# Performance work log

Hardware: AMD Instinct MI355X
Metric: run time of the kernel (lower is better)

The kernel has to match this reference:

```python
import jax, jax.numpy as jnp
import numpy as np

DIM = 768
HEADS = 12
HEAD_DIM = DIM // HEADS
HIDDEN = int(DIM * 4.0)
EPS = 1e-5


def _layernorm(x, g, b):
    mu = jnp.mean(x, axis=-1, keepdims=True)
    var = jnp.var(x, axis=-1, keepdims=True)
    return (x - mu) * jax.lax.rsqrt(var + EPS) * g + b


def setup_inputs() -> dict:
    key = jax.random.key(0)
    ks = jax.random.split(key, 12)
    s = 0.02
    return {
        "x": jax.random.normal(ks[0], (8, 1024, DIM), dtype=jnp.float32),
        "norm1_g": jnp.ones((DIM,), jnp.float32),
        "norm1_b": jnp.zeros((DIM,), jnp.float32),
        "qkv_w": jax.random.normal(ks[1], (3 * DIM, DIM), jnp.float32) * s,
        "qkv_b": jnp.zeros((3 * DIM,), jnp.float32),
        "proj_w": jax.random.normal(ks[2], (DIM, DIM), jnp.float32) * s,
        "proj_b": jnp.zeros((DIM,), jnp.float32),
        "norm2_g": jnp.ones((DIM,), jnp.float32),
        "norm2_b": jnp.zeros((DIM,), jnp.float32),
        "fc1_w": jax.random.normal(ks[3], (HIDDEN, DIM), jnp.float32) * s,
        "fc1_b": jnp.zeros((HIDDEN,), jnp.float32),
        "fc2_w": jax.random.normal(ks[4], (DIM, HIDDEN), jnp.float32) * s,
        "fc2_b": jnp.zeros((DIM,), jnp.float32),
    }


def reference(x, norm1_g, norm1_b, qkv_w, qkv_b, proj_w, proj_b,
              norm2_g, norm2_b, fc1_w, fc1_b, fc2_w, fc2_b):
    B, N, C = x.shape
    scale = HEAD_DIM ** -0.5

    # --- MHSA with pre-norm + residual ---
    h = _layernorm(x, norm1_g, norm1_b)
    qkv = h @ qkv_w.T + qkv_b                      # [B, N, 3C]
    qkv = qkv.reshape(B, N, 3, HEADS, HEAD_DIM)
    qkv = jnp.transpose(qkv, (2, 0, 3, 1, 4))      # [3, B, H, N, Dh]
    q, k, v = qkv[0], qkv[1], qkv[2]
    attn = jnp.einsum("bhnd,bhmd->bhnm", q, k) * scale
    attn = jax.nn.softmax(attn, axis=-1)
    o = jnp.einsum("bhnm,bhmd->bhnd", attn, v)     # [B, H, N, Dh]
    o = jnp.transpose(o, (0, 2, 1, 3)).reshape(B, N, C)
    x = x + (o @ proj_w.T + proj_b)

    # --- MLP with pre-norm + residual ---
    h = _layernorm(x, norm2_g, norm2_b)
    h = jax.nn.gelu(h @ fc1_w.T + fc1_b, approximate=False)
    x = x + (h @ fc2_w.T + fc2_b)
    return x
```

## Files before the change

kernel.cpp:

```cpp
#include <hip/hip_runtime.h>
#include <hip/hip_bf16.h>

typedef unsigned short u16;
using short8  = __attribute__((ext_vector_type(8))) short;
using floatx4 = __attribute__((ext_vector_type(4))) float;

__device__ inline u16 f2bu(float f) {
    __hip_bfloat16 h = __float2bfloat16(f);
    return __builtin_bit_cast(u16, h);
}
__device__ inline float b2f(u16 u) {
    unsigned v = (unsigned)u << 16;
    return __builtin_bit_cast(float, v);
}
__device__ inline float gelu_f(float v) {
    float u = 1.5957691216f * (v + 0.044715f * v * v * v);
    return v / (1.f + __expf(-u));
}

__device__ inline void load16(const u16* g, u16* l) {
    __builtin_amdgcn_global_load_lds(
        (const __attribute__((address_space(1))) void*)g,
        (__attribute__((address_space(3))) void*)l, 16, 0, 0);
}

__global__ void cvt_bf16v(const float4* __restrict__ in, ushort4* __restrict__ out, int n4) {
    int i = blockIdx.x * 256 + threadIdx.x;
    if (i < n4) {
        float4 f = in[i];
        ushort4 r;
        r.x = f2bu(f.x); r.y = f2bu(f.y); r.z = f2bu(f.z); r.w = f2bu(f.w);
        out[i] = r;
    }
}

__global__ __launch_bounds__(256) void layernorm_bf16(
    const float* __restrict__ x, const float* __restrict__ g,
    const float* __restrict__ b, u16* __restrict__ out)
{
    int row = blockIdx.x;
    int tid = threadIdx.x;
    const float* xr = x + (size_t)row * 768;
    float v0 = xr[tid], v1 = xr[tid + 256], v2 = xr[tid + 512];
    float s = v0 + v1 + v2;
    float ss = v0 * v0 + v1 * v1 + v2 * v2;
    for (int off = 1; off < 64; off <<= 1) {
        s  += __shfl_xor(s, off, 64);
        ss += __shfl_xor(ss, off, 64);
    }
    __shared__ float as[4], ass[4];
    int wave = tid >> 6, lane = tid & 63;
    if (lane == 0) { as[wave] = s; ass[wave] = ss; }
    __syncthreads();
    s  = as[0] + as[1] + as[2] + as[3];
    ss = ass[0] + ass[1] + ass[2] + ass[3];
    float mu  = s * (1.0f / 768.0f);
    float var = ss * (1.0f / 768.0f) - mu * mu;
    float rs  = rsqrtf(var + 1e-5f);
    u16* orow = out + (size_t)row * 768;
    orow[tid]       = f2bu((v0 - mu) * rs * g[tid]       + b[tid]);
    orow[tid + 256] = f2bu((v1 - mu) * rs * g[tid + 256] + b[tid + 256]);
    orow[tid + 512] = f2bu((v2 - mu) * rs * g[tid + 512] + b[tid + 512]);
}

__global__ __launch_bounds__(256) void red2(
    const ushort4* __restrict__ P0, const ushort4* __restrict__ P1,
    const float* __restrict__ bias, const float4* __restrict__ res,
    float4* __restrict__ out)
{
    int i = blockIdx.x * 256 + threadIdx.x;
    int col = (i % 192) * 4;
    ushort4 a = P0[i], b = P1[i];
    float4 o = res ? res[i] : out[i];
    o.x += bias[col + 0] + b2f(a.x) + b2f(b.x);
    o.y += bias[col + 1] + b2f(a.y) + b2f(b.y);
    o.z += bias[col + 2] + b2f(a.z) + b2f(b.z);
    o.w += bias[col + 3] + b2f(a.w) + b2f(b.w);
    out[i] = o;
}

__global__ __launch_bounds__(256) void red2_ln(
    const u16* __restrict__ P0, const u16* __restrict__ P1,
    const float* __restrict__ bias, const float* __restrict__ x,
    float* __restrict__ out,
    const float* __restrict__ g, const float* __restrict__ bb,
    u16* __restrict__ h)
{
    int row = blockIdx.x;
    int tid = threadIdx.x;
    size_t base = (size_t)row * 768;
    float v[3];
    float s = 0.f, ss = 0.f;
    #pragma unroll
    for (int j = 0; j < 3; ++j) {
        int col = tid + j * 256;
        size_t idx = base + col;
        float o = x[idx] + bias[col] + b2f(P0[idx]) + b2f(P1[idx]);
        out[idx] = o;
        v[j] = o;
        s += o; ss += o * o;
    }
    for (int off = 1; off < 64; off <<= 1) {
        s  += __shfl_xor(s, off, 64);
        ss += __shfl_xor(ss, off, 64);
    }
    __shared__ float as[4], ass[4];
    int wave = tid >> 6, lane = tid & 63;
    if (lane == 0) { as[wave] = s; ass[wave] = ss; }
    __syncthreads();
    s  = as[0] + as[1] + as[2] + as[3];
    ss = ass[0] + ass[1] + ass[2] + ass[3];
    float mu  = s * (1.0f / 768.0f);
    float var = ss * (1.0f / 768.0f) - mu * mu;
    float rs  = rsqrtf(var + 1e-5f);
    #pragma unroll
    for (int j = 0; j < 3; ++j) {
        int col = tid + j * 256;
        h[base + col] = f2bu((v[j] - mu) * rs * g[col] + bb[col]);
    }
}

__global__ __launch_bounds__(256) void gemm_k64(
    const u16* __restrict__ A, int lda,
    const u16* __restrict__ B, int ldb,
    int K,
    const float* __restrict__ bias,
    const float* __restrict__ res,
    float* __restrict__ outf, u16* __restrict__ outb,
    u16* __restrict__ parts, size_t pstride,
    int ldc, int act, int splits)
{
    __shared__ u16 lsa[128 * 64];
    __shared__ u16 lsb[128 * 64];

    int tid  = threadIdx.x;
    int wave = tid >> 6, lane = tid & 63;
    int quad = lane >> 4, l16 = lane & 15;
    int wrow = (wave >> 1) * 64;
    int wcol = (wave & 1) * 64;

    int gx = gridDim.x;
    int nblk = gx * gridDim.y;
    int flat = blockIdx.y * gx + blockIdx.x;
    int d = (flat & 7) * (nblk >> 3) + (flat >> 3);
    int m0 = (d / gx) * 128, n0 = (d % gx) * 128;

    int Kper = K / splits;
    int kbeg = blockIdx.z * Kper;

    floatx4 acc[4][4];
    for (int i = 0; i < 4; ++i)
        for (int j = 0; j < 4; ++j)
            acc[i][j] = (floatx4){0.f, 0.f, 0.f, 0.f};

    int rsub = lane >> 3;
    int gc   = (lane & 7) ^ rsub;
    const u16* gA[4];
    const u16* gB[4];
    #pragma unroll
    for (int j = 0; j < 4; ++j) {
        int r = (j * 4 + wave) * 8 + rsub;
        gA[j] = A + (size_t)(m0 + r) * lda + kbeg + gc * 8;
        gB[j] = B + (size_t)(n0 + r) * ldb + kbeg + gc * 8;
    }

    int xq0 = ((quad)     ^ (l16 & 7)) * 8;
    int xq1 = ((quad + 4) ^ (l16 & 7)) * 8;

    for (int k0 = 0; k0 < Kper; k0 += 64) {
        __syncthreads();
        #pragma unroll
        for (int j = 0; j < 4; ++j) {
            load16(gA[j], &lsa[(j * 4 + wave) * 512]);
            gA[j] += 64;
        }
        #pragma unroll
        for (int j = 0; j < 4; ++j) {
            load16(gB[j], &lsb[(j * 4 + wave) * 512]);
            gB[j] += 64;
        }
        __syncthreads();

        short8 af[4], bfr[4];
        #pragma unroll
        for (int rb = 0; rb < 4; ++rb) af[rb]  = *(short8*)&lsa[(wrow + rb * 16 + l16) * 64 + xq0];
        #pragma unroll
        for (int cb = 0; cb < 4; ++cb) bfr[cb] = *(short8*)&lsb[(wcol + cb * 16 + l16) * 64 + xq0];
        #pragma unroll
        for (int rb = 0; rb < 4; ++rb)
            #pragma unroll
            for (int cb = 0; cb < 4; ++cb)
                acc[rb][cb] = __builtin_amdgcn_mfma_f32_16x16x32_bf16(af[rb], bfr[cb], acc[rb][cb], 0, 0, 0);
        #pragma unroll
        for (int rb = 0; rb < 4; ++rb) af[rb]  = *(short8*)&lsa[(wrow + rb * 16 + l16) * 64 + xq1];
        #pragma unroll
        for (int cb = 0; cb < 4; ++cb) bfr[cb] = *(short8*)&lsb[(wcol + cb * 16 + l16) * 64 + xq1];
        #pragma unroll
        for (int rb = 0; rb < 4; ++rb)
            #pragma unroll
            for (int cb = 0; cb < 4; ++cb)
                acc[rb][cb] = __builtin_amdgcn_mfma_f32_16x16x32_bf16(af[rb], bfr[cb], acc[rb][cb], 0, 0, 0);
    }

    u16* pdst = (splits > 1) ? parts + (size_t)blockIdx.z * pstride : nullptr;
    #pragma unroll
    for (int rb = 0; rb < 4; ++rb)
        #pragma unroll
        for (int cb = 0; cb < 4; ++cb)
            #pragma unroll
            for (int r = 0; r < 4; ++r) {
                int row = m0 + wrow + rb * 16 + quad * 4 + r;
                int col = n0 + wcol + cb * 16 + l16;
                float v = acc[rb][cb][r];
                if (splits > 1) {
                    pdst[(size_t)row * ldc + col] = f2bu(v);
                } else {
                    v += bias[col];
                    if (res) v += res[(size_t)row * ldc + col];
                    if (act) v = gelu_f(v);
                    if (outf) outf[(size_t)row * ldc + col] = v;
                    else      outb[(size_t)row * ldc + col] = f2bu(v);
                }
            }
}

__global__ __launch_bounds__(256) void attn_fused(
    const u16* __restrict__ qkv, u16* __restrict__ o)
{
    const int N = 1024, C3 = 2304;
    int qb = blockIdx.x;
    int bh = blockIdx.y;
    int b = bh / 12, h = bh % 12;
    int tid = threadIdx.x, wave = tid >> 6, lane = tid & 63;
    int quad = lane >> 4, l16 = lane & 15;

    __shared__ u16 lk[64 * 64];
    __shared__ u16 lvt[64][72];
    __shared__ u16 lp[4][32][72];

    const size_t base = (size_t)b * N * C3;
    int q0 = qb * 128 + wave * 32;

    short8 qa[2][2];
    #pragma unroll
    for (int rb = 0; rb < 2; ++rb)
        #pragma unroll
        for (int ch = 0; ch < 2; ++ch)
            qa[rb][ch] = *(const short8*)&qkv[base + (size_t)(q0 + rb * 16 + l16) * C3 + h * 64 + ch * 32 + quad * 8];

    floatx4 oacc[2][4];
    #pragma unroll
    for (int i = 0; i < 2; ++i)
        #pragma unroll
        for (int j = 0; j < 4; ++j) oacc[i][j] = (floatx4){0.f, 0.f, 0.f, 0.f};
    float lsum[2][4] = {};

    for (int kt = 0; kt < N; kt += 64) {
        __syncthreads();
        #pragma unroll
        for (int i = 0; i < 2; ++i) {
            int idx = i * 2048 + wave * 512 + lane * 8;
            int r = idx >> 6;
            int gc = (lane & 7) ^ (r & 7);
            load16(&qkv[base + (size_t)(kt + r) * C3 + 768 + h * 64 + gc * 8], &lk[idx]);
        }
        {
            int key = tid & 63, dbase = (tid >> 6) * 16;
            const u16* vp = &qkv[base + (size_t)(kt + key) * C3 + 1536 + h * 64 + dbase];
            uint4 vv0 = *(const uint4*)vp;
            uint4 vv1 = *(const uint4*)(vp + 8);
            const u16* e0 = (const u16*)&vv0;
            const u16* e1 = (const u16*)&vv1;
            #pragma unroll
            for (int i = 0; i < 8; ++i) {
                lvt[dbase + i][key]     = e0[i];
                lvt[dbase + 8 + i][key] = e1[i];
            }
        }
        __syncthreads();

        #pragma unroll
        for (int kb = 0; kb < 4; ++kb) {
            int R = kb * 16 + l16;
            short8 b0 = *(short8*)&lk[R * 64 + ((quad ^ (R & 7)) * 8)];
            short8 b1 = *(short8*)&lk[R * 64 + (((quad + 4) ^ (R & 7)) * 8)];
            #pragma unroll
            for (int rb = 0; rb < 2; ++rb) {
                floatx4 c = (floatx4){0.f, 0.f, 0.f, 0.f};
                c = __builtin_amdgcn_mfma_f32_16x16x32_bf16(qa[rb][0], b0, c, 0, 0, 0);
                c = __builtin_amdgcn_mfma_f32_16x16x32_bf16(qa[rb][1], b1, c, 0, 0, 0);
                #pragma unroll
                for (int r = 0; r < 4; ++r) {
                    float p = __expf(c[r] * 0.125f);
                    lsum[rb][r] += p;
                    lp[wave][rb * 16 + quad * 4 + r][kb * 16 + l16] = f2bu(p);
                }
            }
        }

        short8 pa[2][2];
        #pragma unroll
        for (int rb = 0; rb < 2; ++rb) {
            pa[rb][0] = *(short8*)&lp[wave][rb * 16 + l16][quad * 8];
            pa[rb][1] = *(short8*)&lp[wave][rb * 16 + l16][32 + quad * 8];
        }
        #pragma unroll
        for (int db = 0; db < 4; ++db) {
            short8 vb0 = *(short8*)&lvt[db * 16 + l16][quad * 8];
            short8 vb1 = *(short8*)&lvt[db * 16 + l16][32 + quad * 8];
            #pragma unroll
            for (int rb = 0; rb < 2; ++rb) {
                oacc[rb][db] = __builtin_amdgcn_mfma_f32_16x16x32_bf16(pa[rb][0], vb0, oacc[rb][db], 0, 0, 0);
                oacc[rb][db] = __builtin_amdgcn_mfma_f32_16x16x32_bf16(pa[rb][1], vb1, oacc[rb][db], 0, 0, 0);
            }
        }
    }

    #pragma unroll
    for (int rb = 0; rb < 2; ++rb)
        #pragma unroll
        for (int r = 0; r < 4; ++r)
            for (int off = 1; off < 16; off <<= 1)
                lsum[rb][r] += __shfl_xor(lsum[rb][r], off, 64);

    #pragma unroll
    for (int rb = 0; rb < 2; ++rb)
        #pragma unroll
        for (int db = 0; db < 4; ++db)
            #pragma unroll
            for (int r = 0; r < 4; ++r) {
                int row = q0 + rb * 16 + quad * 4 + r;
                int col = h * 64 + db * 16 + l16;
                o[(size_t)(b * N + row) * 768 + col] = f2bu(oacc[rb][db][r] / lsum[rb][r]);
            }
}

extern "C" void kernel_launch(void* const* d_in, const int* in_sizes, int n_in,
                              void* d_out, int out_size, void* d_ws, size_t ws_size,
                              hipStream_t stream) {
    const float* x      = (const float*)d_in[0];
    const float* n1g    = (const float*)d_in[1];
    const float* n1b    = (const float*)d_in[2];
    const float* qkv_w  = (const float*)d_in[3];
    const float* qkv_b  = (const float*)d_in[4];
    const float* proj_w = (const float*)d_in[5];
    const float* proj_b = (const float*)d_in[6];
    const float* n2g    = (const float*)d_in[7];
    const float* n2b    = (const float*)d_in[8];
    const float* fc1_w  = (const float*)d_in[9];
    const float* fc1_b  = (const float*)d_in[10];
    const float* fc2_w  = (const float*)d_in[11];
    const float* fc2_b  = (const float*)d_in[12];
    float* out = (float*)d_out;

    const int T = 8192;
    char* ws = (char*)d_ws;
    u16* w_qkv  = (u16*)ws;               ws += (size_t)2304 * 768 * 2;
    u16* w_proj = (u16*)ws;               ws += (size_t)768 * 768 * 2;
    u16* w_fc1  = (u16*)ws;               ws += (size_t)3072 * 768 * 2;
    u16* w_fc2  = (u16*)ws;               ws += (size_t)768 * 3072 * 2;
    u16* h_buf  = (u16*)ws;               ws += (size_t)T * 768 * 2;
    u16* qkvbuf = (u16*)ws;               ws += (size_t)T * 2304 * 2;
    u16* o_buf  = (u16*)ws;               ws += (size_t)T * 768 * 2;
    u16* pbuf   = (u16*)ws;               ws += (size_t)T * 768 * 2;
    u16* fc1out = qkvbuf;
    bool do_split = (size_t)(ws - (char*)d_ws) <= ws_size;
    size_t pstr = (size_t)(pbuf - h_buf);

    cvt_bf16v<<<dim3(2304 * 768 / 4 / 256), 256, 0, stream>>>((const float4*)qkv_w,  (ushort4*)w_qkv,  2304 * 768 / 4);
    cvt_bf16v<<<dim3(768 * 768 / 4 / 256),  256, 0, stream>>>((const float4*)proj_w, (ushort4*)w_proj, 768 * 768 / 4);
    cvt_bf16v<<<dim3(3072 * 768 / 4 / 256), 256, 0, stream>>>((const float4*)fc1_w,  (ushort4*)w_fc1,  3072 * 768 / 4);
    cvt_bf16v<<<dim3(768 * 3072 / 4 / 256), 256, 0, stream>>>((const float4*)fc2_w,  (ushort4*)w_fc2,  768 * 3072 / 4);

    layernorm_bf16<<<dim3(T), 256, 0, stream>>>(x, n1g, n1b, h_buf);
    gemm_k64<<<dim3(2304 / 128, T / 128), 256, 0, stream>>>(
        h_buf, 768, w_qkv, 768, 768, qkv_b, nullptr, nullptr, qkvbuf, nullptr, 0, 2304, 0, 1);
    attn_fused<<<dim3(8, 96), 256, 0, stream>>>(qkvbuf, o_buf);
    if (do_split) {
        gemm_k64<<<dim3(768 / 128, T / 128, 2), 256, 0, stream>>>(
            o_buf, 768, w_proj, 768, 768, proj_b, nullptr, nullptr, nullptr,
            h_buf, pstr, 768, 0, 2);
        red2_ln<<<dim3(T), 256, 0, stream>>>(
            h_buf, pbuf, proj_b, x, out, n2g, n2b, h_buf);
    } else {
        gemm_k64<<<dim3(768 / 128, T / 128), 256, 0, stream>>>(
            o_buf, 768, w_proj, 768, 768, proj_b, x, out, nullptr, nullptr, 0, 768, 0, 1);
        layernorm_bf16<<<dim3(T), 256, 0, stream>>>(out, n2g, n2b, h_buf);
    }
    gemm_k64<<<dim3(3072 / 128, T / 128), 256, 0, stream>>>(
        h_buf, 768, w_fc1, 768, 768, fc1_b, nullptr, nullptr, fc1out, nullptr, 0, 3072, 1, 1);
    if (do_split) {
        gemm_k64<<<dim3(768 / 128, T / 128, 2), 256, 0, stream>>>(
            fc1out, 3072, w_fc2, 3072, 3072, fc2_b, nullptr, nullptr, nullptr,
            h_buf, pstr, 768, 0, 2);
        red2<<<dim3(T * 768 / 4 / 256), 256, 0, stream>>>(
            (const ushort4*)h_buf, (const ushort4*)pbuf, fc2_b, nullptr, (float4*)out);
    } else {
        gemm_k64<<<dim3(768 / 128, T / 128), 256, 0, stream>>>(
            fc1out, 3072, w_fc2, 3072, 3072, fc2_b, out, out, nullptr, nullptr, 0, 768, 0, 1);
    }
}
```

Measured before the change: 393.6 us.

## Double-buffer LDS tiles in GEMM and attention kernels with MFMA priority hints

Converts the GEMM and fused-attention main loops to a double-buffered LDS scheme: the next K/A/B tile is prefetched asynchronously into the alternate buffer while MFMAs run on the current one, which halves the barriers per iteration. In attention, V is loaded into registers early and transposed into LDS after compute. s_setprio hints are wrapped around the MFMA blocks to favour matrix issue. This doubles LDS usage (GEMM goes to 64KB), which may reduce occupancy, and it adds register pressure for the V prefetch.

```diff
diff --git a/kernel.cpp b/kernel.cpp
--- a/kernel.cpp
+++ b/kernel.cpp
@@ -130,8 +130,8 @@
     u16* __restrict__ parts, size_t pstride,
     int ldc, int act, int splits)
 {
-    __shared__ u16 lsa[128 * 64];
-    __shared__ u16 lsb[128 * 64];
+    __shared__ u16 lsa[2][128 * 64];
+    __shared__ u16 lsb[2][128 * 64];
 
     int tid  = threadIdx.x;
     int wave = tid >> 6, lane = tid & 63;
@@ -167,39 +167,50 @@
     int xq0 = ((quad)     ^ (l16 & 7)) * 8;
     int xq1 = ((quad + 4) ^ (l16 & 7)) * 8;
 
+    #pragma unroll
+    for (int j = 0; j < 4; ++j) { load16(gA[j], &lsa[0][(j * 4 + wave) * 512]); gA[j] += 64; }
+    #pragma unroll
+    for (int j = 0; j < 4; ++j) { load16(gB[j], &lsb[0][(j * 4 + wave) * 512]); gB[j] += 64; }
+    __syncthreads();
+
+    int cur = 0;
     for (int k0 = 0; k0 < Kper; k0 += 64) {
-        __syncthreads();
-        #pragma unroll
-        for (int j = 0; j < 4; ++j) {
-            load16(gA[j], &lsa[(j * 4 + wave) * 512]);
-            gA[j] += 64;
+        int nxt = cur ^ 1;
+        if (k0 + 64 < Kper) {
+            #pragma unroll
+            for (int j = 0; j < 4; ++j) { load16(gA[j], &lsa[nxt][(j * 4 + wave) * 512]); gA[j] += 64; }
+            #pragma unroll
+            for (int j = 0; j < 4; ++j) { load16(gB[j], &lsb[nxt][(j * 4 + wave) * 512]); gB[j] += 64; }
         }
-        #pragma unroll
-        for (int j = 0; j < 4; ++j) {
-            load16(gB[j], &lsb[(j * 4 + wave) * 512]);
-            gB[j] += 64;
-        }
-        __syncthreads();
-
+
+        const u16* la = lsa[cur];
+        const u16* lb = lsb[cur];
         short8 af[4], bfr[4];
         #pragma unroll
-        for (int rb = 0; rb < 4; ++rb) af[rb]  = *(short8*)&lsa[(wrow + rb * 16 + l16) * 64 + xq0];
-        #pragma unroll
-        for (int cb = 0; cb < 4; ++cb) bfr[cb] = *(short8*)&lsb[(wcol + cb * 16 + l16) * 64 + xq0];
+        for (int rb = 0; rb < 4; ++rb) af[rb]  = *(const short8*)&la[(wrow + rb * 16 + l16) * 64 + xq0];
+        #pragma unroll
+        for (int cb = 0; cb < 4; ++cb) bfr[cb] = *(const short8*)&lb[(wcol + cb * 16 + l16) * 64 + xq0];
+        __builtin_amdgcn_s_setprio(1);
         #pragma unroll
         for (int rb = 0; rb < 4; ++rb)
             #pragma unroll
             for (int cb = 0; cb < 4; ++cb)
                 acc[rb][cb] = __builtin_amdgcn_mfma_f32_16x16x32_bf16(af[rb], bfr[cb], acc[rb][cb], 0, 0, 0);
-        #pragma unroll
-        for (int rb = 0; rb < 4; ++rb) af[rb]  = *(short8*)&lsa[(wrow + rb * 16 + l16) * 64 + xq1];
-        #pragma unroll
-        for (int cb = 0; cb < 4; ++cb) bfr[cb] = *(short8*)&lsb[(wcol + cb * 16 + l16) * 64 + xq1];
+        __builtin_amdgcn_s_setprio(0);
+        #pragma unroll
+        for (int rb = 0; rb < 4; ++rb) af[rb]  = *(const short8*)&la[(wrow + rb * 16 + l16) * 64 + xq1];
+        #pragma unroll
+        for (int cb = 0; cb < 4; ++cb) bfr[cb] = *(const short8*)&lb[(wcol + cb * 16 + l16) * 64 + xq1];
+        __builtin_amdgcn_s_setprio(1);
         #pragma unroll
         for (int rb = 0; rb < 4; ++rb)
             #pragma unroll
             for (int cb = 0; cb < 4; ++cb)
                 acc[rb][cb] = __builtin_amdgcn_mfma_f32_16x16x32_bf16(af[rb], bfr[cb], acc[rb][cb], 0, 0, 0);
+        __builtin_amdgcn_s_setprio(0);
+
+        __syncthreads();
+        cur = nxt;
     }
 
     u16* pdst = (splits > 1) ? parts + (size_t)blockIdx.z * pstride : nullptr;
@@ -224,6 +235,37 @@
             }
 }
 
+__device__ inline void attn_stage_k(const u16* __restrict__ qkv, size_t base, int kt,
+                                    int h, int wave, int lane, u16* lkbuf)
+{
+    #pragma unroll
+    for (int i = 0; i < 2; ++i) {
+        int idx = i * 2048 + wave * 512 + lane * 8;
+        int r = idx >> 6;
+        int gc = (lane & 7) ^ (r & 7);
+        load16(&qkv[base + (size_t)(kt + r) * 2304 + 768 + h * 64 + gc * 8], &lkbuf[idx]);
+    }
+}
+__device__ inline void attn_load_v(const u16* __restrict__ qkv, size_t base, int kt,
+                                   int h, int tid, uint4& v0, uint4& v1)
+{
+    int key = tid & 63, dbase = (tid >> 6) * 16;
+    const u16* vp = &qkv[base + (size_t)(kt + key) * 2304 + 1536 + h * 64 + dbase];
+    v0 = *(const uint4*)vp;
+    v1 = *(const uint4*)(vp + 8);
+}
+__device__ inline void attn_write_v(int tid, const uint4& v0, const uint4& v1, u16 (*lvtbuf)[72])
+{
+    int key = tid & 63, dbase = (tid >> 6) * 16;
+    const u16* e0 = (const u16*)&v0;
+    const u16* e1 = (const u16*)&v1;
+    #pragma unroll
+    for (int i = 0; i < 8; ++i) {
+        lvtbuf[dbase + i][key]     = e0[i];
+        lvtbuf[dbase + 8 + i][key] = e1[i];
+    }
+}
+
 __global__ __launch_bounds__(256) void attn_fused(
     const u16* __restrict__ qkv, u16* __restrict__ o)
 {
@@ -234,8 +276,8 @@
     int tid = threadIdx.x, wave = tid >> 6, lane = tid & 63;
     int quad = lane >> 4, l16 = lane & 15;
 
-    __shared__ u16 lk[64 * 64];
-    __shared__ u16 lvt[64][72];
+    __shared__ u16 lk[2][64 * 64];
+    __shared__ u16 lvt[2][64][72];
     __shared__ u16 lp[4][32][72];
 
     const size_t base = (size_t)b * N * C3;
@@ -255,40 +297,37 @@
         for (int j = 0; j < 4; ++j) oacc[i][j] = (floatx4){0.f, 0.f, 0.f, 0.f};
     float lsum[2][4] = {};
 
+    attn_stage_k(qkv, base, 0, h, wave, lane, lk[0]);
+    {
+        uint4 a0, a1;
+        attn_load_v(qkv, base, 0, h, tid, a0, a1);
+        attn_write_v(tid, a0, a1, lvt[0]);
+    }
+    __syncthreads();
+
+    int cur = 0;
     for (int kt = 0; kt < N; kt += 64) {
-        __syncthreads();
-        #pragma unroll
-        for (int i = 0; i < 2; ++i) {
-            int idx = i * 2048 + wave * 512 + lane * 8;
-            int r = idx >> 6;
-            int gc = (lane & 7) ^ (r & 7);
-            load16(&qkv[base + (size_t)(kt + r) * C3 + 768 + h * 64 + gc * 8], &lk[idx]);
+        int nxt = cur ^ 1;
+        bool pf = (kt + 64) < N;
+        uint4 pv0, pv1;
+        if (pf) {
+            attn_stage_k(qkv, base, kt + 64, h, wave, lane, lk[nxt]);
+            attn_load_v(qkv, base, kt + 64, h, tid, pv0, pv1);
         }
-        {
-            int key = tid & 63, dbase = (tid >> 6) * 16;
-            const u16* vp = &qkv[base + (size_t)(kt + key) * C3 + 1536 + h * 64 + dbase];
-            uint4 vv0 = *(const uint4*)vp;
-            uint4 vv1 = *(const uint4*)(vp + 8);
-            const u16* e0 = (const u16*)&vv0;
-            const u16* e1 = (const u16*)&vv1;
-            #pragma unroll
-            for (int i = 0; i < 8; ++i) {
-                lvt[dbase + i][key]     = e0[i];
-                lvt[dbase + 8 + i][key] = e1[i];
-            }
-        }
-        __syncthreads();
-
+
+        const u16* lkc = lk[cur];
         #pragma unroll
         for (int kb = 0; kb < 4; ++kb) {
             int R = kb * 16 + l16;
-            short8 b0 = *(short8*)&lk[R * 64 + ((quad ^ (R & 7)) * 8)];
-            short8 b1 = *(short8*)&lk[R * 64 + (((quad + 4) ^ (R & 7)) * 8)];
+            short8 b0 = *(const short8*)&lkc[R * 64 + ((quad ^ (R & 7)) * 8)];
+            short8 b1 = *(const short8*)&lkc[R * 64 + (((quad + 4) ^ (R & 7)) * 8)];
             #pragma unroll
             for (int rb = 0; rb < 2; ++rb) {
                 floatx4 c = (floatx4){0.f, 0.f, 0.f, 0.f};
+                __builtin_amdgcn_s_setprio(1);
                 c = __builtin_amdgcn_mfma_f32_16x16x32_bf16(qa[rb][0], b0, c, 0, 0, 0);
                 c = __builtin_amdgcn_mfma_f32_16x16x32_bf16(qa[rb][1], b1, c, 0, 0, 0);
+                __builtin_amdgcn_s_setprio(0);
                 #pragma unroll
                 for (int r = 0; r < 4; ++r) {
                     float p = __expf(c[r] * 0.125f);
@@ -301,19 +340,25 @@
         short8 pa[2][2];
         #pragma unroll
         for (int rb = 0; rb < 2; ++rb) {
-            pa[rb][0] = *(short8*)&lp[wave][rb * 16 + l16][quad * 8];
-            pa[rb][1] = *(short8*)&lp[wave][rb * 16 + l16][32 + quad * 8];
+            pa[rb][0] = *(const short8*)&lp[wave][rb * 16 + l16][quad * 8];
+            pa[rb][1] = *(const short8*)&lp[wave][rb * 16 + l16][32 + quad * 8];
         }
         #pragma unroll
         for (int db = 0; db < 4; ++db) {
-            short8 vb0 = *(short8*)&lvt[db * 16 + l16][quad * 8];
-            short8 vb1 = *(short8*)&lvt[db * 16 + l16][32 + quad * 8];
+            short8 vb0 = *(const short8*)&lvt[cur][db * 16 + l16][quad * 8];
+            short8 vb1 = *(const short8*)&lvt[cur][db * 16 + l16][32 + quad * 8];
+            __builtin_amdgcn_s_setprio(1);
             #pragma unroll
             for (int rb = 0; rb < 2; ++rb) {
                 oacc[rb][db] = __builtin_amdgcn_mfma_f32_16x16x32_bf16(pa[rb][0], vb0, oacc[rb][db], 0, 0, 0);
                 oacc[rb][db] = __builtin_amdgcn_mfma_f32_16x16x32_bf16(pa[rb][1], vb1, oacc[rb][db], 0, 0, 0);
             }
+            __builtin_amdgcn_s_setprio(0);
         }
+
+        if (pf) attn_write_v(tid, pv0, pv1, lvt[nxt]);
+        __syncthreads();
+        cur = nxt;
     }
 
     #pragma unroll
```

New measurement: 447.8 us. +13.8%, slower.

## Double-buffer GEMM LDS tiles with K=32 stages and async prefetch

Applied to the files above, without the earlier changes.

The GEMM main loop now uses two LDS buffers with K-step 32 instead of a single K=64 buffer. The next tile is prefetched via global_load_lds while the current tile is consumed, and waits use vmcnt. The LDS layout packs two rows per 64-element line with an XOR swizzle. The goal is to overlap global loads with MFMA work. In exchange there are twice as many loop iterations and barriers, plus more complex LDS address arithmetic.

```diff
diff --git a/kernel.cpp b/kernel.cpp
--- a/kernel.cpp
+++ b/kernel.cpp
@@ -130,8 +130,7 @@
     u16* __restrict__ parts, size_t pstride,
     int ldc, int act, int splits)
 {
-    __shared__ u16 lsa[128 * 64];
-    __shared__ u16 lsb[128 * 64];
+    __shared__ u16 ls[2][2][64 * 64];
 
     int tid  = threadIdx.x;
     int wave = tid >> 6, lane = tid & 63;
@@ -147,60 +146,66 @@
 
     int Kper = K / splits;
     int kbeg = blockIdx.z * Kper;
+    int NT = Kper >> 5;
 
     floatx4 acc[4][4];
     for (int i = 0; i < 4; ++i)
         for (int j = 0; j < 4; ++j)
             acc[i][j] = (floatx4){0.f, 0.f, 0.f, 0.f};
 
-    int rsub = lane >> 3;
-    int gc   = (lane & 7) ^ rsub;
-    const u16* gA[4];
-    const u16* gB[4];
-    #pragma unroll
-    for (int j = 0; j < 4; ++j) {
-        int r = (j * 4 + wave) * 8 + rsub;
-        gA[j] = A + (size_t)(m0 + r) * lda + kbeg + gc * 8;
-        gB[j] = B + (size_t)(n0 + r) * ldb + kbeg + gc * 8;
-    }
-
-    int xq0 = ((quad)     ^ (l16 & 7)) * 8;
-    int xq1 = ((quad + 4) ^ (l16 & 7)) * 8;
-
-    for (int k0 = 0; k0 < Kper; k0 += 64) {
-        __syncthreads();
-        #pragma unroll
-        for (int j = 0; j < 4; ++j) {
-            load16(gA[j], &lsa[(j * 4 + wave) * 512]);
-            gA[j] += 64;
-        }
-        #pragma unroll
-        for (int j = 0; j < 4; ++j) {
-            load16(gB[j], &lsb[(j * 4 + wave) * 512]);
-            gB[j] += 64;
-        }
-        __syncthreads();
-
+    int rsub  = lane >> 3;
+    int gc    = (lane & 7) ^ rsub;
+    int ghalf = gc >> 2, gq = gc & 3;
+    const u16* gA[2];
+    const u16* gB[2];
+    #pragma unroll
+    for (int j = 0; j < 2; ++j) {
+        int r = ((j * 4 + wave) * 8 + rsub) * 2 + ghalf;
+        gA[j] = A + (size_t)(m0 + r) * lda + kbeg + gq * 8;
+        gB[j] = B + (size_t)(n0 + r) * ldb + kbeg + gq * 8;
+    }
+
+#define STAGE(bf_) do { \
+    _Pragma("unroll") \
+    for (int j_ = 0; j_ < 2; ++j_) { load16(gA[j_], &ls[bf_][0][(j_ * 4 + wave) * 512]); gA[j_] += 32; } \
+    _Pragma("unroll") \
+    for (int j_ = 0; j_ < 2; ++j_) { load16(gB[j_], &ls[bf_][1][(j_ * 4 + wave) * 512]); gB[j_] += 32; } \
+} while (0)
+
+    STAGE(0);
+
+    for (int c = 0; c < NT; ++c) {
+        int bc = c & 1;
+        __builtin_amdgcn_s_barrier();
+        if (c + 1 < NT) {
+            STAGE(bc ^ 1);
+            asm volatile("s_waitcnt vmcnt(4)" ::: "memory");
+        } else {
+            asm volatile("s_waitcnt vmcnt(0)" ::: "memory");
+        }
+        __builtin_amdgcn_s_barrier();
+        __builtin_amdgcn_sched_barrier(0);
+
+        const u16* la = ls[bc][0];
+        const u16* lb = ls[bc][1];
         short8 af[4], bfr[4];
         #pragma unroll
-        for (int rb = 0; rb < 4; ++rb) af[rb]  = *(short8*)&lsa[(wrow + rb * 16 + l16) * 64 + xq0];
-        #pragma unroll
-        for (int cb = 0; cb < 4; ++cb) bfr[cb] = *(short8*)&lsb[(wcol + cb * 16 + l16) * 64 + xq0];
+        for (int rb = 0; rb < 4; ++rb) {
+            int r = wrow + rb * 16 + l16;
+            af[rb] = *(const short8*)&la[(r >> 1) * 64 + (((((r & 1) << 2) + quad) ^ ((r >> 1) & 7)) << 3)];
+        }
+        #pragma unroll
+        for (int cb = 0; cb < 4; ++cb) {
+            int r = wcol + cb * 16 + l16;
+            bfr[cb] = *(const short8*)&lb[(r >> 1) * 64 + (((((r & 1) << 2) + quad) ^ ((r >> 1) & 7)) << 3)];
+        }
         #pragma unroll
         for (int rb = 0; rb < 4; ++rb)
             #pragma unroll
             for (int cb = 0; cb < 4; ++cb)
                 acc[rb][cb] = __builtin_amdgcn_mfma_f32_16x16x32_bf16(af[rb], bfr[cb], acc[rb][cb], 0, 0, 0);
-        #pragma unroll
-        for (int rb = 0; rb < 4; ++rb) af[rb]  = *(short8*)&lsa[(wrow + rb * 16 + l16) * 64 + xq1];
-        #pragma unroll
-        for (int cb = 0; cb < 4; ++cb) bfr[cb] = *(short8*)&lsb[(wcol + cb * 16 + l16) * 64 + xq1];
-        #pragma unroll
-        for (int rb = 0; rb < 4; ++rb)
-            #pragma unroll
-            for (int cb = 0; cb < 4; ++cb)
-                acc[rb][cb] = __builtin_amdgcn_mfma_f32_16x16x32_bf16(af[rb], bfr[cb], acc[rb][cb], 0, 0, 0);
-    }
+    }
+#undef STAGE
 
     u16* pdst = (splits > 1) ? parts + (size_t)blockIdx.z * pstride : nullptr;
     #pragma unroll
```

After: 403.8 us. 2.6% more time.
